# Kernel tuning notes

Hardware: AMD Instinct MI355X
Metric: run time of the kernel (lower is better)

## Reference

```python
import jax, jax.numpy as jnp
import numpy as np

B, D, M, H, DK = 8192, 256, 10, 4, 64
LN_EPS = 1e-3  # keras LayerNormalization default


def _layernorm(x, gamma, beta):
    mu = jnp.mean(x, axis=-1, keepdims=True)
    var = jnp.mean(jnp.square(x - mu), axis=-1, keepdims=True)
    return (x - mu) * jax.lax.rsqrt(var + LN_EPS) * gamma + beta


def setup_inputs() -> dict:
    key = jax.random.key(0)
    ks = jax.random.split(key, 16)
    n = lambda k, shp, s=0.02: jax.random.normal(k, shp, dtype=jnp.float32) * s
    return {
        'inputs': jax.random.normal(ks[0], (B, D), dtype=jnp.float32),
        'h_prev': jax.random.normal(ks[1], (B, D), dtype=jnp.float32),
        'memory_flat': jax.random.normal(ks[2], (B, M * D), dtype=jnp.float32),
        'W_in': n(ks[3], (D, D)), 'b_in': jnp.zeros((D,), jnp.float32),
        'gru_k': n(ks[4], (D, 3 * D)), 'gru_rk': n(ks[5], (D, 3 * D)),
        'gru_b': jnp.zeros((2, 3 * D), jnp.float32),
        'Wq': n(ks[6], (D, H, DK)), 'bq': jnp.zeros((H, DK), jnp.float32),
        'Wk': n(ks[7], (D, H, DK)), 'bk': jnp.zeros((H, DK), jnp.float32),
        'Wv': n(ks[8], (D, H, DK)), 'bv': jnp.zeros((H, DK), jnp.float32),
        'Wo': n(ks[9], (H, DK, D)), 'bo': jnp.zeros((D,), jnp.float32),
        'g_attn': jnp.ones((D,), jnp.float32), 'beta_attn': jnp.zeros((D,), jnp.float32),
        'g_out': jnp.ones((D,), jnp.float32), 'beta_out': jnp.zeros((D,), jnp.float32),
        'W_ctx': n(ks[10], (D, D)), 'b_ctx': jnp.zeros((D,), jnp.float32),
        'W_gate': n(ks[11], (2 * D, D)), 'b_gate': jnp.zeros((D,), jnp.float32),
        'W_mem': n(ks[12], (D, D)), 'b_mem': jnp.zeros((D,), jnp.float32),
    }


def reference(inputs, h_prev, memory_flat, W_in, b_in, gru_k, gru_rk, gru_b,
              Wq, bq, Wk, bk, Wv, bv, Wo, bo, g_attn, beta_attn, g_out, beta_out,
              W_ctx, b_ctx, W_gate, b_gate, W_mem, b_mem):
    bsz = inputs.shape[0]
    # input projection
    z_t = inputs @ W_in + b_in                      # (B, D)
    mem = memory_flat.reshape(bsz, M, D)            # (B, M, D)

    # keras GRUCell (reset_after=True)
    xp = z_t @ gru_k + gru_b[0]                     # (B, 3D)
    hp = h_prev @ gru_rk + gru_b[1]                 # (B, 3D)
    xz, xr, xh = jnp.split(xp, 3, axis=-1)
    hz, hr, hh = jnp.split(hp, 3, axis=-1)
    z = jax.nn.sigmoid(xz + hz)
    r = jax.nn.sigmoid(xr + hr)
    hc = jnp.tanh(xh + r * hh)
    gru_out = z * h_prev + (1.0 - z) * hc           # (B, D)

    # multi-head attention: query len 1 over memory of size M
    q = jnp.einsum('bd,dhk->bhk', gru_out, Wq) + bq           # (B, H, DK)
    k = jnp.einsum('bmd,dhk->bmhk', mem, Wk) + bk             # (B, M, H, DK)
    v = jnp.einsum('bmd,dhk->bmhk', mem, Wv) + bv
    scores = jnp.einsum('bhk,bmhk->bhm', q, k) / np.float32(np.sqrt(DK))
    attn = jax.nn.softmax(scores, axis=-1)                    # (B, H, M)
    ctx_h = jnp.einsum('bhm,bmhk->bhk', attn, v)
    context = jnp.einsum('bhk,hkd->bd', ctx_h, Wo) + bo       # (B, D)

    context = _layernorm(context, g_attn, beta_attn)
    ctx_p = jnp.tanh(context @ W_ctx + b_ctx)

    alpha = jax.nn.sigmoid(jnp.concatenate([gru_out, ctx_p], axis=-1) @ W_gate + b_gate)
    h_corr = _layernorm((1.0 - alpha) * gru_out + alpha * ctx_p, g_out, beta_out)

    # memory shift + write
    new_entry = z_t @ W_mem + b_mem                 # (B, D)
    new_mem = jnp.concatenate([mem[:, 1:, :], new_entry[:, None, :]], axis=1)
    new_memory_flat = new_mem.reshape(bsz, M * D)
    return h_corr, new_memory_flat
```

## Files before the change

### kernel.cpp

```cpp
#include <hip/hip_runtime.h>
#include <hip/hip_bf16.h>
#include <cstdint>
#include <cstddef>

#define BN 8192
#define DN 256

typedef short bf16x8 __attribute__((ext_vector_type(8)));
typedef float f32x4 __attribute__((ext_vector_type(4)));

#define O_WINT   0
#define O_GKT    65536
#define O_GRKT   262144
#define O_WQT    458752
#define O_WK     524288
#define O_WVT    589824
#define O_WOT    655360
#define O_WCTXT  720896
#define O_WGT    786432
#define O_WMT    917504
#define W_TOTAL  983040
#define OB_GRUF  ((size_t)(2*1024*1024))
#define OB_QK    ((size_t)(OB_GRUF + 8388608))

__device__ __forceinline__ short f2bf(float x){
  unsigned u = __builtin_bit_cast(unsigned, x);
  u = (u + 0x7fffu + ((u >> 16) & 1u)) >> 16;
  return (short)u;
}
__device__ __forceinline__ float bf2f(short s){
  unsigned u = ((unsigned)(unsigned short)s) << 16;
  return __builtin_bit_cast(float, u);
}
__device__ __forceinline__ float sigm(float x){ return 1.f/(1.f+__expf(-x)); }
__device__ __forceinline__ float tanh_(float x){
  x = fminf(20.f, fmaxf(-20.f, x));
  float e = __expf(-2.f*x);
  return (1.f - e)/(1.f + e);
}
__device__ __forceinline__ f32x4 mfma16(bf16x8 a, bf16x8 b, f32x4 c){
  return __builtin_amdgcn_mfma_f32_16x16x32_bf16(a, b, c, 0, 0, 0);
}
__device__ __forceinline__ bf16x8 frag_f32(const float* p){
  float4 a = *reinterpret_cast<const float4*>(p);
  float4 b = *reinterpret_cast<const float4*>(p+4);
  bf16x8 v;
  v[0]=f2bf(a.x); v[1]=f2bf(a.y); v[2]=f2bf(a.z); v[3]=f2bf(a.w);
  v[4]=f2bf(b.x); v[5]=f2bf(b.y); v[6]=f2bf(b.z); v[7]=f2bf(b.w);
  return v;
}

__global__ __launch_bounds__(256) void k_prep(
    const float* __restrict__ W_in, const float* __restrict__ gru_k,
    const float* __restrict__ gru_rk, const float* __restrict__ Wq,
    const float* __restrict__ Wk, const float* __restrict__ Wv,
    const float* __restrict__ Wo, const float* __restrict__ W_ctx,
    const float* __restrict__ W_gate, const float* __restrict__ W_mem,
    short* __restrict__ wp)
{
  int idx = blockIdx.x*256 + threadIdx.x;
  if (idx < 65536){ int n=idx>>8, k=idx&255; wp[O_WINT+idx]=f2bf(W_in[k*256+n]); return; }
  idx -= 65536;
  if (idx < 196608){ int n=idx>>8, k=idx&255; wp[O_GKT+idx]=f2bf(gru_k[k*768+n]); return; }
  idx -= 196608;
  if (idx < 196608){ int n=idx>>8, k=idx&255; wp[O_GRKT+idx]=f2bf(gru_rk[k*768+n]); return; }
  idx -= 196608;
  if (idx < 65536){ int n=idx>>8, k=idx&255; wp[O_WQT+idx]=f2bf(Wq[k*256+n]); return; }
  idx -= 65536;
  if (idx < 65536){ wp[O_WK+idx]=f2bf(Wk[idx]); return; }
  idx -= 65536;
  if (idx < 65536){ int n=idx>>8, k=idx&255; wp[O_WVT+idx]=f2bf(Wv[k*256+n]); return; }
  idx -= 65536;
  if (idx < 65536){ int n=idx>>8, k=idx&255; wp[O_WOT+idx]=f2bf(Wo[k*256+n]); return; }
  idx -= 65536;
  if (idx < 65536){ int n=idx>>8, k=idx&255; wp[O_WCTXT+idx]=f2bf(W_ctx[k*256+n]); return; }
  idx -= 65536;
  if (idx < 131072){ int n=idx>>9, k=idx&511; wp[O_WGT+idx]=f2bf(W_gate[k*256+n]); return; }
  idx -= 131072;
  if (idx < 65536){ int n=idx>>8, k=idx&255; wp[O_WMT+idx]=f2bf(W_mem[k*256+n]); }
}

__global__ __launch_bounds__(256) void k_gru(
    const float* __restrict__ inputs, const float* __restrict__ h_prev,
    const float* __restrict__ b_in, const float* __restrict__ gru_b,
    const float* __restrict__ bq, const float* __restrict__ b_mem,
    const short* __restrict__ wp,
    float* __restrict__ gruout_f, short* __restrict__ qk_bf,
    float* __restrict__ d_out)
{
  const int tid = threadIdx.x;
  const int wv = tid >> 6, lane = tid & 63;
  const int r16 = lane & 15, kk = (lane >> 4) * 8, vr4 = (lane >> 4) * 4;
  const int row0 = blockIdx.x * 32;
  const int cb = wv * 64;

  __shared__ __attribute__((aligned(16))) short sZ[32*272];
  __shared__ __attribute__((aligned(16))) short sG[32*272];

  {
    f32x4 acc[2][4] = {};
    for (int k0=0; k0<256; k0+=32){
      bf16x8 a[2], b[4];
      #pragma unroll
      for (int rt=0; rt<2; rt++)
        a[rt] = frag_f32(inputs + (size_t)(row0+rt*16+r16)*256 + k0 + kk);
      #pragma unroll
      for (int ct=0; ct<4; ct++)
        b[ct] = *reinterpret_cast<const bf16x8*>(wp + O_WINT + (cb+ct*16+r16)*256 + k0 + kk);
      #pragma unroll
      for (int rt=0; rt<2; rt++)
        #pragma unroll
        for (int ct=0; ct<4; ct++)
          acc[rt][ct] = mfma16(a[rt], b[ct], acc[rt][ct]);
    }
    #pragma unroll
    for (int rt=0; rt<2; rt++)
      #pragma unroll
      for (int ct=0; ct<4; ct++)
        #pragma unroll
        for (int v=0; v<4; v++){
          int lrow = rt*16 + vr4 + v, col = cb + ct*16 + r16;
          sZ[lrow*272 + col] = f2bf(acc[rt][ct][v] + b_in[col]);
        }
  }
  __syncthreads();

  {
    f32x4 acc[2][4] = {};
    for (int k0=0; k0<256; k0+=32){
      bf16x8 a[2], b[4];
      #pragma unroll
      for (int rt=0; rt<2; rt++)
        a[rt] = *reinterpret_cast<const bf16x8*>(sZ + (rt*16+r16)*272 + k0 + kk);
      #pragma unroll
      for (int ct=0; ct<4; ct++)
        b[ct] = *reinterpret_cast<const bf16x8*>(wp + O_WMT + (cb+ct*16+r16)*256 + k0 + kk);
      #pragma unroll
      for (int rt=0; rt<2; rt++)
        #pragma unroll
        for (int ct=0; ct<4; ct++)
          acc[rt][ct] = mfma16(a[rt], b[ct], acc[rt][ct]);
    }
    float* om = d_out + (size_t)BN*256;
    #pragma unroll
    for (int rt=0; rt<2; rt++)
      #pragma unroll
      for (int ct=0; ct<4; ct++)
        #pragma unroll
        for (int v=0; v<4; v++){
          int grow = row0 + rt*16 + vr4 + v, col = cb + ct*16 + r16;
          om[(size_t)grow*2560 + 2304 + col] = acc[rt][ct][v] + b_mem[col];
        }
  }

  for (int ct=0; ct<4; ct++){
    const int c = cb + ct*16;
    f32x4 az[2] = {}, arr[2] = {}, ax[2] = {}, ah[2] = {};
    for (int k0=0; k0<256; k0+=32){
      bf16x8 aZ[2], aH[2];
      #pragma unroll
      for (int rt=0; rt<2; rt++){
        aZ[rt] = *reinterpret_cast<const bf16x8*>(sZ + (rt*16+r16)*272 + k0 + kk);
        aH[rt] = frag_f32(h_prev + (size_t)(row0+rt*16+r16)*256 + k0 + kk);
      }
      bf16x8 bz1 = *reinterpret_cast<const bf16x8*>(wp + O_GKT  + (c      +r16)*256 + k0 + kk);
      bf16x8 br1 = *reinterpret_cast<const bf16x8*>(wp + O_GKT  + (256+c  +r16)*256 + k0 + kk);
      bf16x8 bx1 = *reinterpret_cast<const bf16x8*>(wp + O_GKT  + (512+c  +r16)*256 + k0 + kk);
      bf16x8 bz2 = *reinterpret_cast<const bf16x8*>(wp + O_GRKT + (c      +r16)*256 + k0 + kk);
      bf16x8 br2 = *reinterpret_cast<const bf16x8*>(wp + O_GRKT + (256+c  +r16)*256 + k0 + kk);
      bf16x8 bh2 = *reinterpret_cast<const bf16x8*>(wp + O_GRKT + (512+c  +r16)*256 + k0 + kk);
      #pragma unroll
      for (int rt=0; rt<2; rt++){
        az[rt]  = mfma16(aZ[rt], bz1, az[rt]);  az[rt]  = mfma16(aH[rt], bz2, az[rt]);
        arr[rt] = mfma16(aZ[rt], br1, arr[rt]); arr[rt] = mfma16(aH[rt], br2, arr[rt]);
        ax[rt]  = mfma16(aZ[rt], bx1, ax[rt]);
        ah[rt]  = mfma16(aH[rt], bh2, ah[rt]);
      }
    }
    #pragma unroll
    for (int rt=0; rt<2; rt++)
      #pragma unroll
      for (int v=0; v<4; v++){
        int lrow = rt*16 + vr4 + v, grow = row0 + lrow, col = c + r16;
        float z  = sigm(az[rt][v]  + gru_b[col]     + gru_b[768+col]);
        float r  = sigm(arr[rt][v] + gru_b[256+col] + gru_b[768+256+col]);
        float hc = tanh_(ax[rt][v] + gru_b[512+col] + r*(ah[rt][v] + gru_b[768+512+col]));
        float hp = h_prev[(size_t)grow*256 + col];
        float go = z*hp + (1.f - z)*hc;
        sG[lrow*272 + col] = f2bf(go);
        gruout_f[(size_t)grow*256 + col] = go;
      }
  }
  __syncthreads();

  {
    f32x4 acc[2][4] = {};
    for (int k0=0; k0<256; k0+=32){
      bf16x8 a[2], b[4];
      #pragma unroll
      for (int rt=0; rt<2; rt++)
        a[rt] = *reinterpret_cast<const bf16x8*>(sG + (rt*16+r16)*272 + k0 + kk);
      #pragma unroll
      for (int ct=0; ct<4; ct++)
        b[ct] = *reinterpret_cast<const bf16x8*>(wp + O_WQT + (cb+ct*16+r16)*256 + k0 + kk);
      #pragma unroll
      for (int rt=0; rt<2; rt++)
        #pragma unroll
        for (int ct=0; ct<4; ct++)
          acc[rt][ct] = mfma16(a[rt], b[ct], acc[rt][ct]);
    }
    __syncthreads();
    #pragma unroll
    for (int rt=0; rt<2; rt++)
      #pragma unroll
      for (int ct=0; ct<4; ct++)
        #pragma unroll
        for (int v=0; v<4; v++){
          int lrow = rt*16 + vr4 + v, col = cb + ct*16 + r16;
          sZ[lrow*272 + col] = f2bf(acc[rt][ct][v] + bq[col]);
        }
  }
  __syncthreads();

  for (int nb=0; nb<4; nb++){
    f32x4 acc[2][4] = {};
    for (int k0=0; k0<64; k0+=32){
      bf16x8 a[2], b[4];
      #pragma unroll
      for (int rt=0; rt<2; rt++)
        a[rt] = *reinterpret_cast<const bf16x8*>(sZ + (rt*16+r16)*272 + wv*64 + k0 + kk);
      #pragma unroll
      for (int ct=0; ct<4; ct++)
        b[ct] = *reinterpret_cast<const bf16x8*>(wp + O_WK + (nb*64+ct*16+r16)*256 + wv*64 + k0 + kk);
      #pragma unroll
      for (int rt=0; rt<2; rt++)
        #pragma unroll
        for (int ct=0; ct<4; ct++)
          acc[rt][ct] = mfma16(a[rt], b[ct], acc[rt][ct]);
    }
    #pragma unroll
    for (int rt=0; rt<2; rt++)
      #pragma unroll
      for (int ct=0; ct<4; ct++)
        #pragma unroll
        for (int v=0; v<4; v++){
          int grow = row0 + rt*16 + vr4 + v, d = nb*64 + ct*16 + r16;
          qk_bf[(size_t)grow*1024 + wv*256 + d] = f2bf(acc[rt][ct][v]);
        }
  }
}

__global__ __launch_bounds__(256) void k_attn(
    const float* __restrict__ mem, short* __restrict__ qkwm,
    float* __restrict__ d_out)
{
  const int wv = threadIdx.x >> 6, lane = threadIdx.x & 63;
  const int b = blockIdx.x*4 + wv;
  const float* mrow = mem + (size_t)b*2560;
  float* orow = d_out + (size_t)BN*256 + (size_t)b*2560;

  float qv[4][4];
  #pragma unroll
  for (int h=0; h<4; h++){
    short4 s = *reinterpret_cast<const short4*>(qkwm + (size_t)b*1024 + h*256 + lane*4);
    qv[h][0]=bf2f(s.x); qv[h][1]=bf2f(s.y); qv[h][2]=bf2f(s.z); qv[h][3]=bf2f(s.w);
  }
  float4 mv[10];
  float sc[10][4];
  #pragma unroll
  for (int m=0; m<10; m++){
    mv[m] = *reinterpret_cast<const float4*>(mrow + m*256 + lane*4);
    if (m >= 1) *reinterpret_cast<float4*>(orow + (m-1)*256 + lane*4) = mv[m];
    #pragma unroll
    for (int h=0; h<4; h++){
      float p = qv[h][0]*mv[m].x + qv[h][1]*mv[m].y + qv[h][2]*mv[m].z + qv[h][3]*mv[m].w;
      p += __shfl_xor(p,32); p += __shfl_xor(p,16); p += __shfl_xor(p,8);
      p += __shfl_xor(p,4);  p += __shfl_xor(p,2);  p += __shfl_xor(p,1);
      sc[m][h] = p * 0.125f;
    }
  }
  #pragma unroll
  for (int h=0; h<4; h++){
    float mx = sc[0][h];
    #pragma unroll
    for (int m=1; m<10; m++) mx = fmaxf(mx, sc[m][h]);
    float s = 0.f;
    #pragma unroll
    for (int m=0; m<10; m++){ float e = __expf(sc[m][h]-mx); sc[m][h]=e; s+=e; }
    float inv = 1.f/s;
    #pragma unroll
    for (int m=0; m<10; m++) sc[m][h] *= inv;
  }
  float w4[4][4] = {};
  #pragma unroll
  for (int m=0; m<10; m++)
    #pragma unroll
    for (int h=0; h<4; h++){
      w4[h][0] += sc[m][h]*mv[m].x; w4[h][1] += sc[m][h]*mv[m].y;
      w4[h][2] += sc[m][h]*mv[m].z; w4[h][3] += sc[m][h]*mv[m].w;
    }
  #pragma unroll
  for (int h=0; h<4; h++){
    short4 o; o.x=f2bf(w4[h][0]); o.y=f2bf(w4[h][1]); o.z=f2bf(w4[h][2]); o.w=f2bf(w4[h][3]);
    *reinterpret_cast<short4*>(qkwm + (size_t)b*1024 + h*256 + lane*4) = o;
  }
}

__device__ __forceinline__ void ln_stats(const float* sF, float sPart[32][8][2],
                                         float sMV[32][2], int tid){
  int r = tid>>3, q = tid&7;
  float s1=0.f, s2=0.f;
  const float* p = sF + r*264 + q*32;
  #pragma unroll
  for (int i=0; i<32; i++){ float v=p[i]; s1+=v; s2+=v*v; }
  sPart[r][q][0]=s1; sPart[r][q][1]=s2;
  __syncthreads();
  if (tid < 32){
    float a=0.f, b2=0.f;
    #pragma unroll
    for (int j=0; j<8; j++){ a+=sPart[tid][j][0]; b2+=sPart[tid][j][1]; }
    float mu = a*(1.f/256.f);
    float var = fmaxf(b2*(1.f/256.f) - mu*mu, 0.f);
    sMV[tid][0]=mu; sMV[tid][1]=rsqrtf(var + 1e-3f);
  }
  __syncthreads();
}

__global__ __launch_bounds__(256) void k_out(
    const short* __restrict__ wmem, const short* __restrict__ wp,
    const float* __restrict__ bv, const float* __restrict__ bo,
    const float* __restrict__ g_attn, const float* __restrict__ beta_attn,
    const float* __restrict__ b_ctx, const float* __restrict__ b_gate,
    const float* __restrict__ g_out, const float* __restrict__ beta_out,
    const float* __restrict__ gruout_f, float* __restrict__ d_out)
{
  const int tid = threadIdx.x, wv = tid>>6, lane = tid&63;
  const int r16 = lane&15, kk = (lane>>4)*8, vr4 = (lane>>4)*4;
  const int row0 = blockIdx.x*32, cb = wv*64;
  __shared__ __attribute__((aligned(16))) short sC[32*272];
  __shared__ __attribute__((aligned(16))) float sF[32*264];
  __shared__ __attribute__((aligned(16))) float sPart[32][8][2];
  __shared__ __attribute__((aligned(16))) float sMV[32][2];

  {
    f32x4 acc[2][4] = {};
    for (int k0=0; k0<256; k0+=32){
      bf16x8 a[2], b[4];
      #pragma unroll
      for (int rt=0; rt<2; rt++)
        a[rt] = *reinterpret_cast<const bf16x8*>(wmem + (size_t)(row0+rt*16+r16)*1024 + wv*256 + k0 + kk);
      #pragma unroll
      for (int ct=0; ct<4; ct++)
        b[ct] = *reinterpret_cast<const bf16x8*>(wp + O_WVT + (wv*64+ct*16+r16)*256 + k0 + kk);
      #pragma unroll
      for (int rt=0; rt<2; rt++)
        #pragma unroll
        for (int ct=0; ct<4; ct++)
          acc[rt][ct] = mfma16(a[rt], b[ct], acc[rt][ct]);
    }
    #pragma unroll
    for (int rt=0; rt<2; rt++)
      #pragma unroll
      for (int ct=0; ct<4; ct++)
        #pragma unroll
        for (int v=0; v<4; v++){
          int lrow = rt*16 + vr4 + v, col = wv*64 + ct*16 + r16;
          sC[lrow*272 + col] = f2bf(acc[rt][ct][v] + bv[col]);
        }
  }
  __syncthreads();

  {
    f32x4 acc[2][4] = {};
    for (int k0=0; k0<256; k0+=32){
      bf16x8 a[2], b[4];
      #pragma unroll
      for (int rt=0; rt<2; rt++)
        a[rt] = *reinterpret_cast<const bf16x8*>(sC + (rt*16+r16)*272 + k0 + kk);
      #pragma unroll
      for (int ct=0; ct<4; ct++)
        b[ct] = *reinterpret_cast<const bf16x8*>(wp + O_WOT + (cb+ct*16+r16)*256 + k0 + kk);
      #pragma unroll
      for (int rt=0; rt<2; rt++)
        #pragma unroll
        for (int ct=0; ct<4; ct++)
          acc[rt][ct] = mfma16(a[rt], b[ct], acc[rt][ct]);
    }
    #pragma unroll
    for (int rt=0; rt<2; rt++)
      #pragma unroll
      for (int ct=0; ct<4; ct++)
        #pragma unroll
        for (int v=0; v<4; v++){
          int lrow = rt*16 + vr4 + v, col = cb + ct*16 + r16;
          sF[lrow*264 + col] = acc[rt][ct][v] + bo[col];
        }
  }
  __syncthreads();

  ln_stats(sF, sPart, sMV, tid);
  {
    int r = tid>>3, q = tid&7;
    float mu = sMV[r][0], rs = sMV[r][1];
    for (int i=0; i<32; i++){
      int c = q*32 + i;
      sC[r*272 + c] = f2bf((sF[r*264+c]-mu)*rs*g_attn[c] + beta_attn[c]);
    }
  }
  __syncthreads();

  f32x4 cpv[2][4];
  {
    f32x4 acc[2][4] = {};
    for (int k0=0; k0<256; k0+=32){
      bf16x8 a[2], b[4];
      #pragma unroll
      for (int rt=0; rt<2; rt++)
        a[rt] = *reinterpret_cast<const bf16x8*>(sC + (rt*16+r16)*272 + k0 + kk);
      #pragma unroll
      for (int ct=0; ct<4; ct++)
        b[ct] = *reinterpret_cast<const bf16x8*>(wp + O_WCTXT + (cb+ct*16+r16)*256 + k0 + kk);
      #pragma unroll
      for (int rt=0; rt<2; rt++)
        #pragma unroll
        for (int ct=0; ct<4; ct++)
          acc[rt][ct] = mfma16(a[rt], b[ct], acc[rt][ct]);
    }
    #pragma unroll
    for (int rt=0; rt<2; rt++)
      #pragma unroll
      for (int ct=0; ct<4; ct++)
        #pragma unroll
        for (int v=0; v<4; v++)
          cpv[rt][ct][v] = tanh_(acc[rt][ct][v] + b_ctx[cb + ct*16 + r16]);
  }
  __syncthreads();
  #pragma unroll
  for (int rt=0; rt<2; rt++)
    #pragma unroll
    for (int ct=0; ct<4; ct++)
      #pragma unroll
      for (int v=0; v<4; v++){
        int lrow = rt*16 + vr4 + v, col = cb + ct*16 + r16;
        sC[lrow*272 + col] = f2bf(cpv[rt][ct][v]);
      }
  __syncthreads();

  {
    f32x4 acc[2][4] = {};
    for (int k0=0; k0<512; k0+=32){
      bf16x8 a[2], b[4];
      if (k0 < 256){
        #pragma unroll
        for (int rt=0; rt<2; rt++)
          a[rt] = frag_f32(gruout_f + (size_t)(row0+rt*16+r16)*256 + k0 + kk);
      } else {
        #pragma unroll
        for (int rt=0; rt<2; rt++)
          a[rt] = *reinterpret_cast<const bf16x8*>(sC + (rt*16+r16)*272 + (k0-256) + kk);
      }
      #pragma unroll
      for (int ct=0; ct<4; ct++)
        b[ct] = *reinterpret_cast<const bf16x8*>(wp + O_WGT + (cb+ct*16+r16)*512 + k0 + kk);
      #pragma unroll
      for (int rt=0; rt<2; rt++)
        #pragma unroll
        for (int ct=0; ct<4; ct++)
          acc[rt][ct] = mfma16(a[rt], b[ct], acc[rt][ct]);
    }
    #pragma unroll
    for (int rt=0; rt<2; rt++)
      #pragma unroll
      for (int ct=0; ct<4; ct++)
        #pragma unroll
        for (int v=0; v<4; v++){
          int lrow = rt*16 + vr4 + v, grow = row0 + lrow, col = cb + ct*16 + r16;
          float al = sigm(acc[rt][ct][v] + b_gate[col]);
          float go = gruout_f[(size_t)grow*256 + col];
          sF[lrow*264 + col] = (1.f-al)*go + al*cpv[rt][ct][v];
        }
  }
  __syncthreads();

  ln_stats(sF, sPart, sMV, tid);
  {
    int r = tid>>3, q = tid&7;
    float mu = sMV[r][0], rs = sMV[r][1];
    int grow = row0 + r;
    for (int i=0; i<32; i++){
      int c = q*32 + i;
      d_out[(size_t)grow*256 + c] = (sF[r*264+c]-mu)*rs*g_out[c] + beta_out[c];
    }
  }
}

extern "C" void kernel_launch(void* const* d_in, const int* in_sizes, int n_in,
                              void* d_out, int out_size, void* d_ws, size_t ws_size,
                              hipStream_t stream)
{
  const float* inputs   = (const float*)d_in[0];
  const float* h_prev   = (const float*)d_in[1];
  const float* memory   = (const float*)d_in[2];
  const float* W_in     = (const float*)d_in[3];
  const float* b_in     = (const float*)d_in[4];
  const float* gru_k    = (const float*)d_in[5];
  const float* gru_rk   = (const float*)d_in[6];
  const float* gru_b    = (const float*)d_in[7];
  const float* Wq       = (const float*)d_in[8];
  const float* bq       = (const float*)d_in[9];
  const float* Wk       = (const float*)d_in[10];
  const float* Wv       = (const float*)d_in[12];
  const float* bv       = (const float*)d_in[13];
  const float* Wo       = (const float*)d_in[14];
  const float* bo       = (const float*)d_in[15];
  const float* g_attn   = (const float*)d_in[16];
  const float* beta_attn= (const float*)d_in[17];
  const float* g_out    = (const float*)d_in[18];
  const float* beta_out = (const float*)d_in[19];
  const float* W_ctx    = (const float*)d_in[20];
  const float* b_ctx    = (const float*)d_in[21];
  const float* W_gate   = (const float*)d_in[22];
  const float* b_gate   = (const float*)d_in[23];
  const float* W_mem    = (const float*)d_in[24];
  const float* b_mem    = (const float*)d_in[25];

  short* wp       = (short*)d_ws;
  float* gruout_f = (float*)((char*)d_ws + OB_GRUF);
  short* qkwm     = (short*)((char*)d_ws + OB_QK);
  float* out      = (float*)d_out;

  k_prep<<<W_TOTAL/256, 256, 0, stream>>>(W_in, gru_k, gru_rk, Wq, Wk, Wv, Wo,
                                          W_ctx, W_gate, W_mem, wp);
  k_gru <<<BN/32, 256, 0, stream>>>(inputs, h_prev, b_in, gru_b, bq, b_mem,
                                    wp, gruout_f, qkwm, out);
  k_attn<<<BN/4, 256, 0, stream>>>(memory, qkwm, out);
  k_out <<<BN/32, 256, 0, stream>>>(qkwm, wp, bv, bo, g_attn, beta_attn,
                                    b_ctx, b_gate, g_out, beta_out, gruout_f, out);
}
```

Baseline: 323.3 us.

## Fuse GRU, attention and output stages into one kernel with 16-row tiles

Merges the three kernels (GRU/query, attention over memory, output projection and LayerNorms) into a single kernel that processes 16 rows per block. Intermediates such as gru_out and the q·Wk / weighted-memory vectors now stay in shared memory instead of going through global workspace buffers. The LayerNorm reduction moves to warp shuffles, and the final output store is vectorised. Halving the row tile doubles how often each block reloads weights and leaves fewer MFMAs per weight fragment, in exchange for more blocks and no inter-kernel global traffic.

```diff
diff --git a/kernel.cpp b/kernel.cpp
--- a/kernel.cpp
+++ b/kernel.cpp
@@ -4,7 +4,6 @@
 #include <cstddef>
 
 #define BN 8192
-#define DN 256
 
 typedef short bf16x8 __attribute__((ext_vector_type(8)));
 typedef float f32x4 __attribute__((ext_vector_type(4)));
@@ -20,8 +19,11 @@
 #define O_WGT    786432
 #define O_WMT    917504
 #define W_TOTAL  983040
-#define OB_GRUF  ((size_t)(2*1024*1024))
-#define OB_QK    ((size_t)(OB_GRUF + 8388608))
+
+#define SZS  264
+#define SGOS 260
+#define SQS  1032
+#define SFS  260
 
 __device__ __forceinline__ short f2bf(float x){
   unsigned u = __builtin_bit_cast(unsigned, x);
@@ -80,416 +82,320 @@
   if (idx < 65536){ int n=idx>>8, k=idx&255; wp[O_WMT+idx]=f2bf(W_mem[k*256+n]); }
 }
 
-__global__ __launch_bounds__(256) void k_gru(
+__global__ __launch_bounds__(256) void k_fused(
     const float* __restrict__ inputs, const float* __restrict__ h_prev,
+    const float* __restrict__ mem,
     const float* __restrict__ b_in, const float* __restrict__ gru_b,
     const float* __restrict__ bq, const float* __restrict__ b_mem,
-    const short* __restrict__ wp,
-    float* __restrict__ gruout_f, short* __restrict__ qk_bf,
-    float* __restrict__ d_out)
+    const float* __restrict__ bv, const float* __restrict__ bo,
+    const float* __restrict__ g_attn, const float* __restrict__ beta_attn,
+    const float* __restrict__ b_ctx, const float* __restrict__ b_gate,
+    const float* __restrict__ g_out, const float* __restrict__ beta_out,
+    const short* __restrict__ wp, float* __restrict__ d_out)
 {
   const int tid = threadIdx.x;
   const int wv = tid >> 6, lane = tid & 63;
   const int r16 = lane & 15, kk = (lane >> 4) * 8, vr4 = (lane >> 4) * 4;
-  const int row0 = blockIdx.x * 32;
+  const int row0 = blockIdx.x * 16;
   const int cb = wv * 64;
 
-  __shared__ __attribute__((aligned(16))) short sZ[32*272];
-  __shared__ __attribute__((aligned(16))) short sG[32*272];
-
-  {
-    f32x4 acc[2][4] = {};
-    for (int k0=0; k0<256; k0+=32){
-      bf16x8 a[2], b[4];
-      #pragma unroll
-      for (int rt=0; rt<2; rt++)
-        a[rt] = frag_f32(inputs + (size_t)(row0+rt*16+r16)*256 + k0 + kk);
-      #pragma unroll
-      for (int ct=0; ct<4; ct++)
-        b[ct] = *reinterpret_cast<const bf16x8*>(wp + O_WINT + (cb+ct*16+r16)*256 + k0 + kk);
-      #pragma unroll
-      for (int rt=0; rt<2; rt++)
-        #pragma unroll
-        for (int ct=0; ct<4; ct++)
-          acc[rt][ct] = mfma16(a[rt], b[ct], acc[rt][ct]);
-    }
-    #pragma unroll
-    for (int rt=0; rt<2; rt++)
-      #pragma unroll
-      for (int ct=0; ct<4; ct++)
-        #pragma unroll
-        for (int v=0; v<4; v++){
-          int lrow = rt*16 + vr4 + v, col = cb + ct*16 + r16;
-          sZ[lrow*272 + col] = f2bf(acc[rt][ct][v] + b_in[col]);
-        }
-  }
-  __syncthreads();
-
-  {
-    f32x4 acc[2][4] = {};
-    for (int k0=0; k0<256; k0+=32){
-      bf16x8 a[2], b[4];
-      #pragma unroll
-      for (int rt=0; rt<2; rt++)
-        a[rt] = *reinterpret_cast<const bf16x8*>(sZ + (rt*16+r16)*272 + k0 + kk);
-      #pragma unroll
-      for (int ct=0; ct<4; ct++)
-        b[ct] = *reinterpret_cast<const bf16x8*>(wp + O_WMT + (cb+ct*16+r16)*256 + k0 + kk);
-      #pragma unroll
-      for (int rt=0; rt<2; rt++)
-        #pragma unroll
-        for (int ct=0; ct<4; ct++)
-          acc[rt][ct] = mfma16(a[rt], b[ct], acc[rt][ct]);
+  __shared__ __attribute__((aligned(16))) short sZ[16*SZS];
+  __shared__ __attribute__((aligned(16))) float sGO[16*SGOS];
+  __shared__ __attribute__((aligned(16))) short sQK[16*SQS];
+  float* sF = (float*)sQK;
+
+  {
+    f32x4 acc[4] = {};
+    for (int k0=0; k0<256; k0+=32){
+      bf16x8 a = frag_f32(inputs + (size_t)(row0+r16)*256 + k0 + kk);
+      #pragma unroll
+      for (int ct=0; ct<4; ct++){
+        bf16x8 b = *reinterpret_cast<const bf16x8*>(wp + O_WINT + (cb+ct*16+r16)*256 + k0 + kk);
+        acc[ct] = mfma16(a, b, acc[ct]);
+      }
+    }
+    #pragma unroll
+    for (int ct=0; ct<4; ct++)
+      #pragma unroll
+      for (int v=0; v<4; v++){
+        int col = cb + ct*16 + r16;
+        sZ[(vr4+v)*SZS + col] = f2bf(acc[ct][v] + b_in[col]);
+      }
+  }
+  __syncthreads();
+
+  {
+    f32x4 acc[4] = {};
+    for (int k0=0; k0<256; k0+=32){
+      bf16x8 a = *reinterpret_cast<const bf16x8*>(sZ + r16*SZS + k0 + kk);
+      #pragma unroll
+      for (int ct=0; ct<4; ct++){
+        bf16x8 b = *reinterpret_cast<const bf16x8*>(wp + O_WMT + (cb+ct*16+r16)*256 + k0 + kk);
+        acc[ct] = mfma16(a, b, acc[ct]);
+      }
     }
     float* om = d_out + (size_t)BN*256;
     #pragma unroll
-    for (int rt=0; rt<2; rt++)
-      #pragma unroll
-      for (int ct=0; ct<4; ct++)
-        #pragma unroll
-        for (int v=0; v<4; v++){
-          int grow = row0 + rt*16 + vr4 + v, col = cb + ct*16 + r16;
-          om[(size_t)grow*2560 + 2304 + col] = acc[rt][ct][v] + b_mem[col];
-        }
-  }
-
+    for (int ct=0; ct<4; ct++)
+      #pragma unroll
+      for (int v=0; v<4; v++){
+        int col = cb + ct*16 + r16;
+        om[(size_t)(row0+vr4+v)*2560 + 2304 + col] = acc[ct][v] + b_mem[col];
+      }
+  }
+
+  #pragma unroll
   for (int ct=0; ct<4; ct++){
     const int c = cb + ct*16;
-    f32x4 az[2] = {}, arr[2] = {}, ax[2] = {}, ah[2] = {};
-    for (int k0=0; k0<256; k0+=32){
-      bf16x8 aZ[2], aH[2];
-      #pragma unroll
-      for (int rt=0; rt<2; rt++){
-        aZ[rt] = *reinterpret_cast<const bf16x8*>(sZ + (rt*16+r16)*272 + k0 + kk);
-        aH[rt] = frag_f32(h_prev + (size_t)(row0+rt*16+r16)*256 + k0 + kk);
-      }
+    f32x4 az = {}, arr = {}, ax = {}, ah = {};
+    for (int k0=0; k0<256; k0+=32){
+      bf16x8 aZ = *reinterpret_cast<const bf16x8*>(sZ + r16*SZS + k0 + kk);
+      bf16x8 aH = frag_f32(h_prev + (size_t)(row0+r16)*256 + k0 + kk);
       bf16x8 bz1 = *reinterpret_cast<const bf16x8*>(wp + O_GKT  + (c      +r16)*256 + k0 + kk);
       bf16x8 br1 = *reinterpret_cast<const bf16x8*>(wp + O_GKT  + (256+c  +r16)*256 + k0 + kk);
       bf16x8 bx1 = *reinterpret_cast<const bf16x8*>(wp + O_GKT  + (512+c  +r16)*256 + k0 + kk);
       bf16x8 bz2 = *reinterpret_cast<const bf16x8*>(wp + O_GRKT + (c      +r16)*256 + k0 + kk);
       bf16x8 br2 = *reinterpret_cast<const bf16x8*>(wp + O_GRKT + (256+c  +r16)*256 + k0 + kk);
       bf16x8 bh2 = *reinterpret_cast<const bf16x8*>(wp + O_GRKT + (512+c  +r16)*256 + k0 + kk);
-      #pragma unroll
-      for (int rt=0; rt<2; rt++){
-        az[rt]  = mfma16(aZ[rt], bz1, az[rt]);  az[rt]  = mfma16(aH[rt], bz2, az[rt]);
-        arr[rt] = mfma16(aZ[rt], br1, arr[rt]); arr[rt] = mfma16(aH[rt], br2, arr[rt]);
-        ax[rt]  = mfma16(aZ[rt], bx1, ax[rt]);
-        ah[rt]  = mfma16(aH[rt], bh2, ah[rt]);
-      }
-    }
-    #pragma unroll
-    for (int rt=0; rt<2; rt++)
-      #pragma unroll
-      for (int v=0; v<4; v++){
-        int lrow = rt*16 + vr4 + v, grow = row0 + lrow, col = c + r16;
-        float z  = sigm(az[rt][v]  + gru_b[col]     + gru_b[768+col]);
-        float r  = sigm(arr[rt][v] + gru_b[256+col] + gru_b[768+256+col]);
-        float hc = tanh_(ax[rt][v] + gru_b[512+col] + r*(ah[rt][v] + gru_b[768+512+col]));
-        float hp = h_prev[(size_t)grow*256 + col];
-        float go = z*hp + (1.f - z)*hc;
-        sG[lrow*272 + col] = f2bf(go);
-        gruout_f[(size_t)grow*256 + col] = go;
-      }
-  }
-  __syncthreads();
-
-  {
-    f32x4 acc[2][4] = {};
-    for (int k0=0; k0<256; k0+=32){
-      bf16x8 a[2], b[4];
-      #pragma unroll
-      for (int rt=0; rt<2; rt++)
-        a[rt] = *reinterpret_cast<const bf16x8*>(sG + (rt*16+r16)*272 + k0 + kk);
-      #pragma unroll
-      for (int ct=0; ct<4; ct++)
-        b[ct] = *reinterpret_cast<const bf16x8*>(wp + O_WQT + (cb+ct*16+r16)*256 + k0 + kk);
-      #pragma unroll
-      for (int rt=0; rt<2; rt++)
-        #pragma unroll
-        for (int ct=0; ct<4; ct++)
-          acc[rt][ct] = mfma16(a[rt], b[ct], acc[rt][ct]);
+      az  = mfma16(aZ, bz1, az);  az  = mfma16(aH, bz2, az);
+      arr = mfma16(aZ, br1, arr); arr = mfma16(aH, br2, arr);
+      ax  = mfma16(aZ, bx1, ax);
+      ah  = mfma16(aH, bh2, ah);
+    }
+    #pragma unroll
+    for (int v=0; v<4; v++){
+      int lrow = vr4 + v, grow = row0 + lrow, col = c + r16;
+      float z  = sigm(az[v]  + gru_b[col]     + gru_b[768+col]);
+      float r  = sigm(arr[v] + gru_b[256+col] + gru_b[768+256+col]);
+      float hc = tanh_(ax[v] + gru_b[512+col] + r*(ah[v] + gru_b[768+512+col]));
+      float hp = h_prev[(size_t)grow*256 + col];
+      sGO[lrow*SGOS + col] = z*hp + (1.f - z)*hc;
+    }
+  }
+  __syncthreads();
+
+  {
+    f32x4 acc[4] = {};
+    for (int k0=0; k0<256; k0+=32){
+      bf16x8 a = frag_f32(sGO + r16*SGOS + k0 + kk);
+      #pragma unroll
+      for (int ct=0; ct<4; ct++){
+        bf16x8 b = *reinterpret_cast<const bf16x8*>(wp + O_WQT + (cb+ct*16+r16)*256 + k0 + kk);
+        acc[ct] = mfma16(a, b, acc[ct]);
+      }
+    }
+    #pragma unroll
+    for (int ct=0; ct<4; ct++)
+      #pragma unroll
+      for (int v=0; v<4; v++){
+        int col = cb + ct*16 + r16;
+        sZ[(vr4+v)*SZS + col] = f2bf(acc[ct][v] + bq[col]);
+      }
+  }
+  __syncthreads();
+
+  for (int nb=0; nb<4; nb++){
+    f32x4 acc[4] = {};
+    #pragma unroll
+    for (int k0=0; k0<64; k0+=32){
+      bf16x8 a = *reinterpret_cast<const bf16x8*>(sZ + r16*SZS + wv*64 + k0 + kk);
+      #pragma unroll
+      for (int ct=0; ct<4; ct++){
+        bf16x8 b = *reinterpret_cast<const bf16x8*>(wp + O_WK + (nb*64+ct*16+r16)*256 + wv*64 + k0 + kk);
+        acc[ct] = mfma16(a, b, acc[ct]);
+      }
+    }
+    #pragma unroll
+    for (int ct=0; ct<4; ct++)
+      #pragma unroll
+      for (int v=0; v<4; v++){
+        int d = nb*64 + ct*16 + r16;
+        sQK[(vr4+v)*SQS + wv*256 + d] = f2bf(acc[ct][v]);
+      }
+  }
+  __syncthreads();
+
+  for (int i=0; i<4; i++){
+    const int rr = wv*4 + i;
+    const float* mrow = mem + (size_t)(row0+rr)*2560;
+    float* orow = d_out + (size_t)BN*256 + (size_t)(row0+rr)*2560;
+
+    float qv[4][4];
+    #pragma unroll
+    for (int h=0; h<4; h++){
+      short4 s = *reinterpret_cast<const short4*>(sQK + rr*SQS + h*256 + lane*4);
+      qv[h][0]=bf2f(s.x); qv[h][1]=bf2f(s.y); qv[h][2]=bf2f(s.z); qv[h][3]=bf2f(s.w);
+    }
+    float4 mv[10];
+    float sc[10][4];
+    #pragma unroll
+    for (int m=0; m<10; m++){
+      mv[m] = *reinterpret_cast<const float4*>(mrow + m*256 + lane*4);
+      if (m >= 1) *reinterpret_cast<float4*>(orow + (m-1)*256 + lane*4) = mv[m];
+      #pragma unroll
+      for (int h=0; h<4; h++){
+        float p = qv[h][0]*mv[m].x + qv[h][1]*mv[m].y + qv[h][2]*mv[m].z + qv[h][3]*mv[m].w;
+        p += __shfl_xor(p,32); p += __shfl_xor(p,16); p += __shfl_xor(p,8);
+        p += __shfl_xor(p,4);  p += __shfl_xor(p,2);  p += __shfl_xor(p,1);
+        sc[m][h] = p * 0.125f;
+      }
+    }
+    #pragma unroll
+    for (int h=0; h<4; h++){
+      float mx = sc[0][h];
+      #pragma unroll
+      for (int m=1; m<10; m++) mx = fmaxf(mx, sc[m][h]);
+      float s = 0.f;
+      #pragma unroll
+      for (int m=0; m<10; m++){ float e = __expf(sc[m][h]-mx); sc[m][h]=e; s+=e; }
+      float inv = 1.f/s;
+      #pragma unroll
+      for (int m=0; m<10; m++) sc[m][h] *= inv;
+    }
+    float w4[4][4] = {};
+    #pragma unroll
+    for (int m=0; m<10; m++)
+      #pragma unroll
+      for (int h=0; h<4; h++){
+        w4[h][0] += sc[m][h]*mv[m].x; w4[h][1] += sc[m][h]*mv[m].y;
+        w4[h][2] += sc[m][h]*mv[m].z; w4[h][3] += sc[m][h]*mv[m].w;
+      }
+    #pragma unroll
+    for (int h=0; h<4; h++){
+      short4 o; o.x=f2bf(w4[h][0]); o.y=f2bf(w4[h][1]); o.z=f2bf(w4[h][2]); o.w=f2bf(w4[h][3]);
+      *reinterpret_cast<short4*>(sQK + rr*SQS + h*256 + lane*4) = o;
+    }
+  }
+  __syncthreads();
+
+  {
+    f32x4 acc[4] = {};
+    for (int k0=0; k0<256; k0+=32){
+      bf16x8 a = *reinterpret_cast<const bf16x8*>(sQK + r16*SQS + wv*256 + k0 + kk);
+      #pragma unroll
+      for (int ct=0; ct<4; ct++){
+        bf16x8 b = *reinterpret_cast<const bf16x8*>(wp + O_WVT + (cb+ct*16+r16)*256 + k0 + kk);
+        acc[ct] = mfma16(a, b, acc[ct]);
+      }
+    }
+    #pragma unroll
+    for (int ct=0; ct<4; ct++)
+      #pragma unroll
+      for (int v=0; v<4; v++){
+        int col = cb + ct*16 + r16;
+        sZ[(vr4+v)*SZS + col] = f2bf(acc[ct][v] + bv[col]);
+      }
+  }
+  __syncthreads();
+
+  {
+    f32x4 acc[4] = {};
+    for (int k0=0; k0<256; k0+=32){
+      bf16x8 a = *reinterpret_cast<const bf16x8*>(sZ + r16*SZS + k0 + kk);
+      #pragma unroll
+      for (int ct=0; ct<4; ct++){
+        bf16x8 b = *reinterpret_cast<const bf16x8*>(wp + O_WOT + (cb+ct*16+r16)*256 + k0 + kk);
+        acc[ct] = mfma16(a, b, acc[ct]);
+      }
     }
     __syncthreads();
     #pragma unroll
-    for (int rt=0; rt<2; rt++)
-      #pragma unroll
-      for (int ct=0; ct<4; ct++)
-        #pragma unroll
-        for (int v=0; v<4; v++){
-          int lrow = rt*16 + vr4 + v, col = cb + ct*16 + r16;
-          sZ[lrow*272 + col] = f2bf(acc[rt][ct][v] + bq[col]);
-        }
-  }
-  __syncthreads();
-
-  for (int nb=0; nb<4; nb++){
-    f32x4 acc[2][4] = {};
-    for (int k0=0; k0<64; k0+=32){
-      bf16x8 a[2], b[4];
-      #pragma unroll
-      for (int rt=0; rt<2; rt++)
-        a[rt] = *reinterpret_cast<const bf16x8*>(sZ + (rt*16+r16)*272 + wv*64 + k0 + kk);
-      #pragma unroll
-      for (int ct=0; ct<4; ct++)
-        b[ct] = *reinterpret_cast<const bf16x8*>(wp + O_WK + (nb*64+ct*16+r16)*256 + wv*64 + k0 + kk);
-      #pragma unroll
-      for (int rt=0; rt<2; rt++)
-        #pragma unroll
-        for (int ct=0; ct<4; ct++)
-          acc[rt][ct] = mfma16(a[rt], b[ct], acc[rt][ct]);
-    }
-    #pragma unroll
-    for (int rt=0; rt<2; rt++)
-      #pragma unroll
-      for (int ct=0; ct<4; ct++)
-        #pragma unroll
-        for (int v=0; v<4; v++){
-          int grow = row0 + rt*16 + vr4 + v, d = nb*64 + ct*16 + r16;
-          qk_bf[(size_t)grow*1024 + wv*256 + d] = f2bf(acc[rt][ct][v]);
-        }
-  }
-}
-
-__global__ __launch_bounds__(256) void k_attn(
-    const float* __restrict__ mem, short* __restrict__ qkwm,
-    float* __restrict__ d_out)
-{
-  const int wv = threadIdx.x >> 6, lane = threadIdx.x & 63;
-  const int b = blockIdx.x*4 + wv;
-  const float* mrow = mem + (size_t)b*2560;
-  float* orow = d_out + (size_t)BN*256 + (size_t)b*2560;
-
-  float qv[4][4];
+    for (int ct=0; ct<4; ct++)
+      #pragma unroll
+      for (int v=0; v<4; v++){
+        int col = cb + ct*16 + r16;
+        sF[(vr4+v)*SFS + col] = acc[ct][v] + bo[col];
+      }
+  }
+  __syncthreads();
+
+  {
+    int r = tid >> 4, q = tid & 15;
+    float s1=0.f, s2=0.f;
+    #pragma unroll
+    for (int ii=0; ii<16; ii++){ float v = sF[r*SFS + q*16 + ii]; s1+=v; s2+=v*v; }
+    #pragma unroll
+    for (int off=8; off; off>>=1){ s1 += __shfl_xor(s1,off); s2 += __shfl_xor(s2,off); }
+    float mu = s1*(1.f/256.f);
+    float rs = rsqrtf(fmaxf(s2*(1.f/256.f) - mu*mu, 0.f) + 1e-3f);
+    #pragma unroll
+    for (int ii=0; ii<16; ii++){
+      int c = q*16 + ii;
+      sZ[r*SZS + c] = f2bf((sF[r*SFS + c]-mu)*rs*g_attn[c] + beta_attn[c]);
+    }
+  }
+  __syncthreads();
+
+  f32x4 cpv[4];
+  {
+    f32x4 acc[4] = {};
+    for (int k0=0; k0<256; k0+=32){
+      bf16x8 a = *reinterpret_cast<const bf16x8*>(sZ + r16*SZS + k0 + kk);
+      #pragma unroll
+      for (int ct=0; ct<4; ct++){
+        bf16x8 b = *reinterpret_cast<const bf16x8*>(wp + O_WCTXT + (cb+ct*16+r16)*256 + k0 + kk);
+        acc[ct] = mfma16(a, b, acc[ct]);
+      }
+    }
+    #pragma unroll
+    for (int ct=0; ct<4; ct++)
+      #pragma unroll
+      for (int v=0; v<4; v++)
+        cpv[ct][v] = tanh_(acc[ct][v] + b_ctx[cb + ct*16 + r16]);
+  }
+  __syncthreads();
   #pragma unroll
-  for (int h=0; h<4; h++){
-    short4 s = *reinterpret_cast<const short4*>(qkwm + (size_t)b*1024 + h*256 + lane*4);
-    qv[h][0]=bf2f(s.x); qv[h][1]=bf2f(s.y); qv[h][2]=bf2f(s.z); qv[h][3]=bf2f(s.w);
-  }
-  float4 mv[10];
-  float sc[10][4];
-  #pragma unroll
-  for (int m=0; m<10; m++){
-    mv[m] = *reinterpret_cast<const float4*>(mrow + m*256 + lane*4);
-    if (m >= 1) *reinterpret_cast<float4*>(orow + (m-1)*256 + lane*4) = mv[m];
-    #pragma unroll
-    for (int h=0; h<4; h++){
-      float p = qv[h][0]*mv[m].x + qv[h][1]*mv[m].y + qv[h][2]*mv[m].z + qv[h][3]*mv[m].w;
-      p += __shfl_xor(p,32); p += __shfl_xor(p,16); p += __shfl_xor(p,8);
-      p += __shfl_xor(p,4);  p += __shfl_xor(p,2);  p += __shfl_xor(p,1);
-      sc[m][h] = p * 0.125f;
-    }
-  }
-  #pragma unroll
-  for (int h=0; h<4; h++){
-    float mx = sc[0][h];
-    #pragma unroll
-    for (int m=1; m<10; m++) mx = fmaxf(mx, sc[m][h]);
-    float s = 0.f;
-    #pragma unroll
-    for (int m=0; m<10; m++){ float e = __expf(sc[m][h]-mx); sc[m][h]=e; s+=e; }
-    float inv = 1.f/s;
-    #pragma unroll
-    for (int m=0; m<10; m++) sc[m][h] *= inv;
-  }
-  float w4[4][4] = {};
-  #pragma unroll
-  for (int m=0; m<10; m++)
-    #pragma unroll
-    for (int h=0; h<4; h++){
-      w4[h][0] += sc[m][h]*mv[m].x; w4[h][1] += sc[m][h]*mv[m].y;
-      w4[h][2] += sc[m][h]*mv[m].z; w4[h][3] += sc[m][h]*mv[m].w;
-    }
-  #pragma unroll
-  for (int h=0; h<4; h++){
-    short4 o; o.x=f2bf(w4[h][0]); o.y=f2bf(w4[h][1]); o.z=f2bf(w4[h][2]); o.w=f2bf(w4[h][3]);
-    *reinterpret_cast<short4*>(qkwm + (size_t)b*1024 + h*256 + lane*4) = o;
-  }
-}
-
-__device__ __forceinline__ void ln_stats(const float* sF, float sPart[32][8][2],
-                                         float sMV[32][2], int tid){
-  int r = tid>>3, q = tid&7;
-  float s1=0.f, s2=0.f;
-  const float* p = sF + r*264 + q*32;
-  #pragma unroll
-  for (int i=0; i<32; i++){ float v=p[i]; s1+=v; s2+=v*v; }
-  sPart[r][q][0]=s1; sPart[r][q][1]=s2;
-  __syncthreads();
-  if (tid < 32){
-    float a=0.f, b2=0.f;
-    #pragma unroll
-    for (int j=0; j<8; j++){ a+=sPart[tid][j][0]; b2+=sPart[tid][j][1]; }
-    float mu = a*(1.f/256.f);
-    float var = fmaxf(b2*(1.f/256.f) - mu*mu, 0.f);
-    sMV[tid][0]=mu; sMV[tid][1]=rsqrtf(var + 1e-3f);
-  }
-  __syncthreads();
-}
-
-__global__ __launch_bounds__(256) void k_out(
-    const short* __restrict__ wmem, const short* __restrict__ wp,
-    const float* __restrict__ bv, const float* __restrict__ bo,
-    const float* __restrict__ g_attn, const float* __restrict__ beta_attn,
-    const float* __restrict__ b_ctx, const float* __restrict__ b_gate,
-    const float* __restrict__ g_out, const float* __restrict__ beta_out,
-    const float* __restrict__ gruout_f, float* __restrict__ d_out)
-{
-  const int tid = threadIdx.x, wv = tid>>6, lane = tid&63;
-  const int r16 = lane&15, kk = (lane>>4)*8, vr4 = (lane>>4)*4;
-  const int row0 = blockIdx.x*32, cb = wv*64;
-  __shared__ __attribute__((aligned(16))) short sC[32*272];
-  __shared__ __attribute__((aligned(16))) float sF[32*264];
-  __shared__ __attribute__((aligned(16))) float sPart[32][8][2];
-  __shared__ __attribute__((aligned(16))) float sMV[32][2];
-
-  {
-    f32x4 acc[2][4] = {};
-    for (int k0=0; k0<256; k0+=32){
-      bf16x8 a[2], b[4];
-      #pragma unroll
-      for (int rt=0; rt<2; rt++)
-        a[rt] = *reinterpret_cast<const bf16x8*>(wmem + (size_t)(row0+rt*16+r16)*1024 + wv*256 + k0 + kk);
-      #pragma unroll
-      for (int ct=0; ct<4; ct++)
-        b[ct] = *reinterpret_cast<const bf16x8*>(wp + O_WVT + (wv*64+ct*16+r16)*256 + k0 + kk);
-      #pragma unroll
-      for (int rt=0; rt<2; rt++)
-        #pragma unroll
-        for (int ct=0; ct<4; ct++)
-          acc[rt][ct] = mfma16(a[rt], b[ct], acc[rt][ct]);
-    }
-    #pragma unroll
-    for (int rt=0; rt<2; rt++)
-      #pragma unroll
-      for (int ct=0; ct<4; ct++)
-        #pragma unroll
-        for (int v=0; v<4; v++){
-          int lrow = rt*16 + vr4 + v, col = wv*64 + ct*16 + r16;
-          sC[lrow*272 + col] = f2bf(acc[rt][ct][v] + bv[col]);
-        }
-  }
-  __syncthreads();
-
-  {
-    f32x4 acc[2][4] = {};
-    for (int k0=0; k0<256; k0+=32){
-      bf16x8 a[2], b[4];
-      #pragma unroll
-      for (int rt=0; rt<2; rt++)
-        a[rt] = *reinterpret_cast<const bf16x8*>(sC + (rt*16+r16)*272 + k0 + kk);
-      #pragma unroll
-      for (int ct=0; ct<4; ct++)
-        b[ct] = *reinterpret_cast<const bf16x8*>(wp + O_WOT + (cb+ct*16+r16)*256 + k0 + kk);
-      #pragma unroll
-      for (int rt=0; rt<2; rt++)
-        #pragma unroll
-        for (int ct=0; ct<4; ct++)
-          acc[rt][ct] = mfma16(a[rt], b[ct], acc[rt][ct]);
-    }
-    #pragma unroll
-    for (int rt=0; rt<2; rt++)
-      #pragma unroll
-      for (int ct=0; ct<4; ct++)
-        #pragma unroll
-        for (int v=0; v<4; v++){
-          int lrow = rt*16 + vr4 + v, col = cb + ct*16 + r16;
-          sF[lrow*264 + col] = acc[rt][ct][v] + bo[col];
-        }
-  }
-  __syncthreads();
-
-  ln_stats(sF, sPart, sMV, tid);
-  {
-    int r = tid>>3, q = tid&7;
-    float mu = sMV[r][0], rs = sMV[r][1];
-    for (int i=0; i<32; i++){
-      int c = q*32 + i;
-      sC[r*272 + c] = f2bf((sF[r*264+c]-mu)*rs*g_attn[c] + beta_attn[c]);
-    }
-  }
-  __syncthreads();
-
-  f32x4 cpv[2][4];
-  {
-    f32x4 acc[2][4] = {};
-    for (int k0=0; k0<256; k0+=32){
-      bf16x8 a[2], b[4];
-      #pragma unroll
-      for (int rt=0; rt<2; rt++)
-        a[rt] = *reinterpret_cast<const bf16x8*>(sC + (rt*16+r16)*272 + k0 + kk);
-      #pragma unroll
-      for (int ct=0; ct<4; ct++)
-        b[ct] = *reinterpret_cast<const bf16x8*>(wp + O_WCTXT + (cb+ct*16+r16)*256 + k0 + kk);
-      #pragma unroll
-      for (int rt=0; rt<2; rt++)
-        #pragma unroll
-        for (int ct=0; ct<4; ct++)
-          acc[rt][ct] = mfma16(a[rt], b[ct], acc[rt][ct]);
-    }
-    #pragma unroll
-    for (int rt=0; rt<2; rt++)
-      #pragma unroll
-      for (int ct=0; ct<4; ct++)
-        #pragma unroll
-        for (int v=0; v<4; v++)
-          cpv[rt][ct][v] = tanh_(acc[rt][ct][v] + b_ctx[cb + ct*16 + r16]);
-  }
-  __syncthreads();
-  #pragma unroll
-  for (int rt=0; rt<2; rt++)
-    #pragma unroll
-    for (int ct=0; ct<4; ct++)
-      #pragma unroll
-      for (int v=0; v<4; v++){
-        int lrow = rt*16 + vr4 + v, col = cb + ct*16 + r16;
-        sC[lrow*272 + col] = f2bf(cpv[rt][ct][v]);
-      }
-  __syncthreads();
-
-  {
-    f32x4 acc[2][4] = {};
+  for (int ct=0; ct<4; ct++)
+    #pragma unroll
+    for (int v=0; v<4; v++){
+      int col = cb + ct*16 + r16;
+      sZ[(vr4+v)*SZS + col] = f2bf(cpv[ct][v]);
+    }
+  __syncthreads();
+
+  {
+    f32x4 acc[4] = {};
     for (int k0=0; k0<512; k0+=32){
-      bf16x8 a[2], b[4];
-      if (k0 < 256){
-        #pragma unroll
-        for (int rt=0; rt<2; rt++)
-          a[rt] = frag_f32(gruout_f + (size_t)(row0+rt*16+r16)*256 + k0 + kk);
-      } else {
-        #pragma unroll
-        for (int rt=0; rt<2; rt++)
-          a[rt] = *reinterpret_cast<const bf16x8*>(sC + (rt*16+r16)*272 + (k0-256) + kk);
-      }
-      #pragma unroll
-      for (int ct=0; ct<4; ct++)
-        b[ct] = *reinterpret_cast<const bf16x8*>(wp + O_WGT + (cb+ct*16+r16)*512 + k0 + kk);
-      #pragma unroll
-      for (int rt=0; rt<2; rt++)
-        #pragma unroll
-        for (int ct=0; ct<4; ct++)
-          acc[rt][ct] = mfma16(a[rt], b[ct], acc[rt][ct]);
-    }
-    #pragma unroll
-    for (int rt=0; rt<2; rt++)
-      #pragma unroll
-      for (int ct=0; ct<4; ct++)
-        #pragma unroll
-        for (int v=0; v<4; v++){
-          int lrow = rt*16 + vr4 + v, grow = row0 + lrow, col = cb + ct*16 + r16;
-          float al = sigm(acc[rt][ct][v] + b_gate[col]);
-          float go = gruout_f[(size_t)grow*256 + col];
-          sF[lrow*264 + col] = (1.f-al)*go + al*cpv[rt][ct][v];
-        }
-  }
-  __syncthreads();
-
-  ln_stats(sF, sPart, sMV, tid);
-  {
-    int r = tid>>3, q = tid&7;
-    float mu = sMV[r][0], rs = sMV[r][1];
-    int grow = row0 + r;
-    for (int i=0; i<32; i++){
-      int c = q*32 + i;
-      d_out[(size_t)grow*256 + c] = (sF[r*264+c]-mu)*rs*g_out[c] + beta_out[c];
+      bf16x8 a;
+      if (k0 < 256) a = frag_f32(sGO + r16*SGOS + k0 + kk);
+      else          a = *reinterpret_cast<const bf16x8*>(sZ + r16*SZS + (k0-256) + kk);
+      #pragma unroll
+      for (int ct=0; ct<4; ct++){
+        bf16x8 b = *reinterpret_cast<const bf16x8*>(wp + O_WGT + (cb+ct*16+r16)*512 + k0 + kk);
+        acc[ct] = mfma16(a, b, acc[ct]);
+      }
+    }
+    #pragma unroll
+    for (int ct=0; ct<4; ct++)
+      #pragma unroll
+      for (int v=0; v<4; v++){
+        int lrow = vr4 + v, col = cb + ct*16 + r16;
+        float al = sigm(acc[ct][v] + b_gate[col]);
+        float go = sGO[lrow*SGOS + col];
+        sF[lrow*SFS + col] = (1.f-al)*go + al*cpv[ct][v];
+      }
+  }
+  __syncthreads();
+
+  {
+    int r = tid >> 4, q = tid & 15;
+    float s1=0.f, s2=0.f;
+    #pragma unroll
+    for (int ii=0; ii<16; ii++){ float v = sF[r*SFS + q*16 + ii]; s1+=v; s2+=v*v; }
+    #pragma unroll
+    for (int off=8; off; off>>=1){ s1 += __shfl_xor(s1,off); s2 += __shfl_xor(s2,off); }
+    float mu = s1*(1.f/256.f);
+    float rs = rsqrtf(fmaxf(s2*(1.f/256.f) - mu*mu, 0.f) + 1e-3f);
+    float* od = d_out + (size_t)(row0+r)*256;
+    #pragma unroll
+    for (int ii=0; ii<16; ii+=4){
+      float4 o;
+      int c = q*16 + ii;
+      o.x = (sF[r*SFS+c+0]-mu)*rs*g_out[c+0] + beta_out[c+0];
+      o.y = (sF[r*SFS+c+1]-mu)*rs*g_out[c+1] + beta_out[c+1];
+      o.z = (sF[r*SFS+c+2]-mu)*rs*g_out[c+2] + beta_out[c+2];
+      o.w = (sF[r*SFS+c+3]-mu)*rs*g_out[c+3] + beta_out[c+3];
+      *reinterpret_cast<float4*>(od + c) = o;
     }
   }
 }
@@ -524,16 +430,13 @@
   const float* W_mem    = (const float*)d_in[24];
   const float* b_mem    = (const float*)d_in[25];
 
-  short* wp       = (short*)d_ws;
-  float* gruout_f = (float*)((char*)d_ws + OB_GRUF);
-  short* qkwm     = (short*)((char*)d_ws + OB_QK);
-  float* out      = (float*)d_out;
+  short* wp  = (short*)d_ws;
+  float* out = (float*)d_out;
 
   k_prep<<<W_TOTAL/256, 256, 0, stream>>>(W_in, gru_k, gru_rk, Wq, Wk, Wv, Wo,
                                           W_ctx, W_gate, W_mem, wp);
-  k_gru <<<BN/32, 256, 0, stream>>>(inputs, h_prev, b_in, gru_b, bq, b_mem,
-                                    wp, gruout_f, qkwm, out);
-  k_attn<<<BN/4, 256, 0, stream>>>(memory, qkwm, out);
-  k_out <<<BN/32, 256, 0, stream>>>(qkwm, wp, bv, bo, g_attn, beta_attn,
-                                    b_ctx, b_gate, g_out, beta_out, gruout_f, out);
-}
+  k_fused<<<BN/16, 256, 0, stream>>>(inputs, h_prev, memory,
+                                     b_in, gru_b, bq, b_mem, bv, bo,
+                                     g_attn, beta_attn, b_ctx, b_gate,
+                                     g_out, beta_out, wp, out);
+}
```

Result: slower. 359.6 us (+11.2%).
